# Optimization experiments

Hardware: AMD Instinct MI355X
Metric: run time of the kernel (lower is better)

Reference implementation:

```python
import jax, jax.numpy as jnp
import numpy as np

VOCAB, EMB, HID = 100000, 300, 600
B, S, N = 256, 64, 64
MAX_LEVEL = 3  # depth of the fixed 4-ary tree


def _tree():
    parent = np.zeros(N, np.int32)
    level = np.zeros(N, np.int32)
    for i in range(1, N):
        parent[i] = (i - 1) // 4
        level[i] = level[parent[i]] + 1
    return parent, level


def setup_inputs() -> dict:
    key = jax.random.key(0)
    ks = jax.random.split(key, 16)
    parent, level = _tree()
    E_tab = jax.random.normal(ks[0], (VOCAB, EMB), jnp.float32) * 0.1
    E_tab = E_tab.at[0].set(0.0)  # padding_idx=0
    return dict(
        premise_x=jax.random.randint(ks[1], (B, S), 0, VOCAB),
        hypothesis_x=jax.random.randint(ks[2], (B, S), 0, VOCAB),
        p_word_idx=jax.random.randint(ks[3], (B, N), -1, S),  # -1 => ones vector
        p_rel_id=jax.random.randint(ks[4], (B, N), -1, 4),    # 0..2 transformed, -1/3 identity
        h_word_idx=jax.random.randint(ks[5], (B, N), -1, S),
        h_rel_id=jax.random.randint(ks[6], (B, N), -1, 4),
        parent=jnp.asarray(parent),
        level=jnp.asarray(level),
        E_tab=E_tab,
        W_enc=jax.random.normal(ks[7], (3, EMB, EMB), jnp.float32) * 0.1,
        W0_w=jax.random.normal(ks[8], (HID, 6 * EMB), jnp.float32) * 0.1,
        W0_b=jax.random.normal(ks[9], (HID,), jnp.float32) * 0.1,
        W1_w=jax.random.normal(ks[10], (HID, HID), jnp.float32) * 0.1,
        W1_b=jax.random.normal(ks[11], (HID,), jnp.float32) * 0.1,
        W2_w=jax.random.normal(ks[12], (HID, HID), jnp.float32) * 0.1,
        W2_b=jax.random.normal(ks[13], (HID,), jnp.float32) * 0.1,
        Wout_w=jax.random.normal(ks[14], (3, HID), jnp.float32) * 0.1,
        Wout_b=jax.random.normal(ks[15], (3,), jnp.float32) * 0.1,
    )


def _encode_sg(seq, word_idx, rel_id, parent, level, W_enc):
    # Level-synchronous bottom-up evaluation of: leaf -> word,
    # internal -> relu(word * mean(rel-transformed children)).
    Bn, Nn = word_idx.shape
    Ed = seq.shape[-1]
    idx = jnp.clip(word_idx, 0, None)
    word = jnp.take_along_axis(seq, idx[:, :, None], axis=1)        # [B,N,E]
    word = jnp.where((word_idx == -1)[..., None], 1.0, word)        # word_idx==-1 => ones
    h = word
    pflat = (parent[None, :] + (jnp.arange(Bn) * Nn)[:, None]).reshape(-1)
    for l in range(MAX_LEVEL, 0, -1):
        is_child = jnp.broadcast_to(level[None, :] == l, (Bn, Nn))
        # per-relation linear W_enc[r]: h @ W.T (torch Linear, no bias)
        t_all = jnp.einsum('bne,rfe->bnrf', h, W_enc)               # [B,N,3,E]
        sel = jnp.clip(rel_id, 0, 2)[:, :, None, None]
        t = jnp.take_along_axis(t_all, sel, axis=2)[:, :, 0, :]
        t = jnp.where(((rel_id >= 0) & (rel_id <= 2))[..., None], t, h)
        contrib = jnp.where(is_child[..., None], t, 0.0).reshape(Bn * Nn, Ed)
        sums = jnp.zeros((Bn * Nn, Ed), h.dtype).at[pflat].add(contrib)
        counts = jnp.zeros((Bn * Nn,), h.dtype).at[pflat].add(
            is_child.astype(h.dtype).reshape(-1))
        mean = (sums / jnp.maximum(counts, 1.0)[:, None]).reshape(Bn, Nn, Ed)
        has_child = (counts.reshape(Bn, Nn) > 0)
        h = jnp.where(has_child[..., None], jax.nn.relu(word * mean), h)
    return h[:, 0, :]  # root representation


def reference(premise_x, hypothesis_x, p_word_idx, p_rel_id, h_word_idx, h_rel_id,
              parent, level, E_tab, W_enc, W0_w, W0_b, W1_w, W1_b, W2_w, W2_b,
              Wout_w, Wout_b):
    emb_p = E_tab[premise_x]      # [B,S,E]
    emb_h = E_tab[hypothesis_x]
    p_rep = emb_p.sum(axis=1)
    h_rep = emb_h.sum(axis=1)
    p_sg = _encode_sg(emb_p, p_word_idx, p_rel_id, parent, level, W_enc)
    h_sg = _encode_sg(emb_h, h_word_idx, h_rel_id, parent, level, W_enc)
    x = jnp.concatenate([p_rep, h_rep, p_rep - h_rep, p_rep * h_rep,
                         p_sg - h_sg, p_sg * h_sg], axis=1)  # [B,6E]
    h1 = jax.nn.relu(x @ W0_w.T + W0_b)
    h2 = jax.nn.relu(h1 @ W1_w.T + W1_b)
    h3 = jax.nn.relu(h2 @ W2_w.T + W2_b)
    return h3 @ Wout_w.T + Wout_b  # [B,3]
```

## Files before the change

kernel.cpp:

```cpp
#include <hip/hip_runtime.h>

constexpr int NB = 256;
constexpr int NS = 64;
constexpr int NN = 64;
constexpr int NE = 300;
constexpr int NH = 600;

typedef __attribute__((ext_vector_type(8))) short bf16x8;
typedef __attribute__((ext_vector_type(4))) float f32x4;

constexpr int KT0 = 57;
constexpr int KT1 = 19;
constexpr int NJT = 40;
constexpr int HP  = 640;

constexpr size_t OFF_REP = 0;
constexpr size_t SZ_REP  = (size_t)2*NB*NE;
constexpr size_t OFF_ROOT= OFF_REP + SZ_REP;
constexpr size_t OFF_WBF = OFF_ROOT + SZ_REP;
constexpr size_t SZ_WBF  = (size_t)3*20*10*64*8/2;
constexpr size_t OFF_W0S = OFF_WBF + SZ_WBF;
constexpr size_t SZ_W0S  = (size_t)KT0*NJT*64*8/2;
constexpr size_t OFF_W1S = OFF_W0S + SZ_W0S;
constexpr size_t SZ_W1S  = (size_t)KT1*NJT*64*8/2;
constexpr size_t OFF_W2S = OFF_W1S + SZ_W1S;
constexpr size_t OFF_XSW = OFF_W2S + SZ_W1S;
constexpr size_t SZ_XSW  = (size_t)KT0*16*64*8/2;
constexpr size_t OFF_H1  = OFF_XSW + SZ_XSW;
constexpr size_t SZ_H    = (size_t)NB*HP/2;
constexpr size_t OFF_H2  = OFF_H1 + SZ_H;
constexpr size_t OFF_H3  = OFF_H2 + SZ_H;

__device__ __forceinline__ ushort f2bf(float x) {
  unsigned u = __float_as_uint(x);
  unsigned r = (u + 0x7FFFu + ((u >> 16) & 1u)) >> 16;
  return (ushort)r;
}
__device__ __forceinline__ float bf2f(ushort u) {
  return __uint_as_float(((unsigned)u) << 16);
}

constexpr int NSWZ = 3*20*10*64;
constexpr int N0S  = KT0*NJT*64;
constexpr int N1S  = KT1*NJT*64;
constexpr int SETUP_ITEMS  = NSWZ + N0S + 2*N1S;
constexpr int SETUP_BLOCKS = SETUP_ITEMS/256;

__global__ __launch_bounds__(256)
void k_setup(const float* __restrict__ Wenc, const float* __restrict__ W0,
             const float* __restrict__ W1, const float* __restrict__ W2,
             ushort* __restrict__ Wbf, ushort* __restrict__ W0S,
             ushort* __restrict__ W1S, ushort* __restrict__ W2S) {
  int t = blockIdx.x*256 + threadIdx.x;
  if (t < NSWZ) {
    int lane = t & 63, rest = t >> 6;
    int ksi = rest % 10, rnt = rest / 10, nt = rnt % 20, r = rnt / 20;
    int f = nt*16 + (lane & 15), e0 = ksi*32 + (lane >> 4)*8;
    ushort v[8];
    #pragma unroll
    for (int j = 0; j < 8; j++) {
      int e = e0 + j;
      v[j] = (f < NE && e < NE) ? f2bf(Wenc[((size_t)r*NE + f)*NE + e]) : (ushort)0;
    }
    *reinterpret_cast<int4*>(&Wbf[(size_t)t*8]) = *reinterpret_cast<const int4*>(v);
    return;
  }
  t -= NSWZ;
  const float* W; ushort* D; int K;
  if (t < N0S)              { W = W0; D = W0S; K = 6*NE; }
  else { t -= N0S;
    if (t < N1S)            { W = W1; D = W1S; K = NH; }
    else { t -= N1S;          W = W2; D = W2S; K = NH; } }
  int lane = t & 63, g = t >> 6;
  int jt = g % NJT, kt = g / NJT;
  int j  = jt*16 + (lane & 15);
  int kb = kt*32 + (lane >> 4)*8;
  ushort v[8];
  #pragma unroll
  for (int i = 0; i < 8; i++) {
    int k = kb + i;
    v[i] = (j < NH && k < K) ? f2bf(W[(size_t)j*K + k]) : (ushort)0;
  }
  *reinterpret_cast<int4*>(&D[(size_t)t*8]) = *reinterpret_cast<const int4*>(v);
}

constexpr int TS = 328;

__global__ __launch_bounds__(256)
void k_tree(const int* __restrict__ px, const int* __restrict__ hx,
            const int* __restrict__ pwi, const int* __restrict__ prel,
            const int* __restrict__ hwi, const int* __restrict__ hrel,
            const float* __restrict__ Etab, const ushort* __restrict__ Wbf,
            float* __restrict__ rep, float* __restrict__ root) {
  __shared__ __align__(16) ushort hS[64*TS];
  __shared__ int xsh[64];
  __shared__ int wish[64];
  __shared__ int relsh[64];
  const int sb = blockIdx.x;
  const int s = sb >> 8, b = sb & 255;
  const int tid = threadIdx.x;

  if (tid < 64) xsh[tid] = ((s ? hx : px) + b*NS)[tid];
  else if (tid < 128) wish[tid-64] = ((s ? hwi : pwi) + b*NN)[tid-64];
  else if (tid < 192) relsh[tid-128] = ((s ? hrel : prel) + b*NN)[tid-128];
  __syncthreads();

  for (int e = tid; e < NE; e += 256) {
    float acc = 0.f;
    #pragma unroll 8
    for (int j = 0; j < NS; j++) acc += Etab[(size_t)xsh[j]*NE + e];
    rep[(size_t)sb*NE + e] = acc;
  }
  for (int flat = tid; flat < 64*75; flat += 256) {
    int n = flat / 75, c = flat % 75;
    int w = wish[n];
    float4 v;
    if (w < 0) v = float4{1.f,1.f,1.f,1.f};
    else v = *reinterpret_cast<const float4*>(&Etab[(size_t)xsh[w]*NE + c*4]);
    ushort4 o; o.x = f2bf(v.x); o.y = f2bf(v.y); o.z = f2bf(v.z); o.w = f2bf(v.w);
    *reinterpret_cast<ushort4*>(&hS[n*TS + c*4]) = o;
  }
  for (int z = tid; z < 64*10; z += 256) {
    int row = z / 10, cc = z % 10;
    *reinterpret_cast<unsigned*>(&hS[row*TS + 300 + cc*2]) = 0u;
  }
  __syncthreads();

  const int wave = tid >> 6, lane = tid & 63;
  const int mrow = lane & 15, quad = lane >> 4;

  {
    const int mb0 = 21, mb1 = 37, mb2 = 53;
    bf16x8 af[3][10];
    #pragma unroll
    for (int ks = 0; ks < 10; ks++) {
      af[0][ks] = *reinterpret_cast<const bf16x8*>(&hS[(mb0+mrow)*TS + ks*32 + quad*8]);
      af[1][ks] = *reinterpret_cast<const bf16x8*>(&hS[(mb1+mrow)*TS + ks*32 + quad*8]);
      int r2 = min(mb2+mrow, 63);
      af[2][ks] = *reinterpret_cast<const bf16x8*>(&hS[r2*TS + ks*32 + quad*8]);
    }
    __syncthreads();
    for (int pr = wave; pr < 57; pr += 4) {
      int r = pr / 19, nt = pr % 19;
      const ushort* Wb = &Wbf[(size_t)((r*20 + nt)*10)*64*8];
      f32x4 acc0 = f32x4{0.f,0.f,0.f,0.f};
      f32x4 acc1 = f32x4{0.f,0.f,0.f,0.f};
      f32x4 acc2 = f32x4{0.f,0.f,0.f,0.f};
      #pragma unroll
      for (int ks = 0; ks < 10; ks++) {
        bf16x8 bf = *reinterpret_cast<const bf16x8*>(&Wb[((size_t)ks*64 + lane)*8]);
        acc0 = __builtin_amdgcn_mfma_f32_16x16x32_bf16(af[0][ks], bf, acc0, 0, 0, 0);
        acc1 = __builtin_amdgcn_mfma_f32_16x16x32_bf16(af[1][ks], bf, acc1, 0, 0, 0);
        acc2 = __builtin_amdgcn_mfma_f32_16x16x32_bf16(af[2][ks], bf, acc2, 0, 0, 0);
      }
      int f = nt*16 + mrow;
      if (f < NE) {
        #pragma unroll
        for (int reg = 0; reg < 4; reg++) {
          int m = quad*4 + reg;
          int c0 = mb0 + m, c1 = mb1 + m, c2 = mb2 + m;
          if (relsh[c0] == r) hS[c0*TS + f] = f2bf(acc0[reg]);
          if (relsh[c1] == r) hS[c1*TS + f] = f2bf(acc1[reg]);
          if (c2 < 64 && relsh[c2] == r) hS[c2*TS + f] = f2bf(acc2[reg]);
        }
      }
    }
    __syncthreads();
    for (int f = tid; f < NE; f += 256) {
      #pragma unroll
      for (int p = 5; p <= 15; p++) {
        int nc = (p == 15) ? 3 : 4;
        float sum = 0.f;
        for (int j = 0; j < nc; j++) sum += bf2f(hS[(4*p+1+j)*TS + f]);
        float v = bf2f(hS[p*TS + f]) * sum * (1.0f/(float)nc);
        hS[p*TS + f] = f2bf(v > 0.f ? v : 0.f);
      }
    }
    __syncthreads();
  }

  {
    bf16x8 af[10];
    #pragma unroll
    for (int ks = 0; ks < 10; ks++)
      af[ks] = *reinterpret_cast<const bf16x8*>(&hS[(5+mrow)*TS + ks*32 + quad*8]);
    __syncthreads();
    for (int pr = wave; pr < 57; pr += 4) {
      int r = pr / 19, nt = pr % 19;
      const ushort* Wb = &Wbf[(size_t)((r*20 + nt)*10)*64*8];
      f32x4 acc = f32x4{0.f,0.f,0.f,0.f};
      #pragma unroll
      for (int ks = 0; ks < 10; ks++) {
        bf16x8 bf = *reinterpret_cast<const bf16x8*>(&Wb[((size_t)ks*64 + lane)*8]);
        acc = __builtin_amdgcn_mfma_f32_16x16x32_bf16(af[ks], bf, acc, 0, 0, 0);
      }
      int f = nt*16 + mrow;
      if (f < NE) {
        #pragma unroll
        for (int reg = 0; reg < 4; reg++) {
          int c = 5 + quad*4 + reg;
          if (relsh[c] == r) hS[c*TS + f] = f2bf(acc[reg]);
        }
      }
    }
    __syncthreads();
    for (int f = tid; f < NE; f += 256) {
      #pragma unroll
      for (int p = 1; p <= 4; p++) {
        float sum = 0.f;
        #pragma unroll
        for (int j = 0; j < 4; j++) sum += bf2f(hS[(4*p+1+j)*TS + f]);
        float v = bf2f(hS[p*TS + f]) * sum * 0.25f;
        hS[p*TS + f] = f2bf(v > 0.f ? v : 0.f);
      }
    }
    __syncthreads();
  }

  {
    bool rp0 = (relsh[1]==0)|(relsh[2]==0)|(relsh[3]==0)|(relsh[4]==0);
    bool rp1 = (relsh[1]==1)|(relsh[2]==1)|(relsh[3]==1)|(relsh[4]==1);
    bool rp2 = (relsh[1]==2)|(relsh[2]==2)|(relsh[3]==2)|(relsh[4]==2);
    bf16x8 af[10];
    #pragma unroll
    for (int ks = 0; ks < 10; ks++)
      af[ks] = *reinterpret_cast<const bf16x8*>(&hS[(1+min(mrow,3))*TS + ks*32 + quad*8]);
    __syncthreads();
    for (int pr = wave; pr < 57; pr += 4) {
      int r = pr / 19, nt = pr % 19;
      if ((r==0 && !rp0) || (r==1 && !rp1) || (r==2 && !rp2)) continue;
      const ushort* Wb = &Wbf[(size_t)((r*20 + nt)*10)*64*8];
      f32x4 acc = f32x4{0.f,0.f,0.f,0.f};
      #pragma unroll
      for (int ks = 0; ks < 10; ks++) {
        bf16x8 bf = *reinterpret_cast<const bf16x8*>(&Wb[((size_t)ks*64 + lane)*8]);
        acc = __builtin_amdgcn_mfma_f32_16x16x32_bf16(af[ks], bf, acc, 0, 0, 0);
      }
      int f = nt*16 + mrow;
      if (f < NE) {
        #pragma unroll
        for (int reg = 0; reg < 4; reg++) {
          int m = quad*4 + reg;
          if (m < 4 && relsh[1+m] == r) hS[(1+m)*TS + f] = f2bf(acc[reg]);
        }
      }
    }
    __syncthreads();
    for (int f = tid; f < NE; f += 256) {
      float sum = 0.f;
      #pragma unroll
      for (int c = 1; c <= 4; c++) sum += bf2f(hS[c*TS + f]);
      float v = bf2f(hS[0*TS + f]) * sum * 0.25f;
      root[(size_t)sb*NE + f] = v > 0.f ? v : 0.f;
    }
  }
}

constexpr int FEAT_ITEMS  = KT0*16*64;
constexpr int FEAT_BLOCKS = FEAT_ITEMS/256;

__global__ __launch_bounds__(256)
void k_feat(const float* __restrict__ rep, const float* __restrict__ root,
            ushort* __restrict__ Xsw) {
  int t = blockIdx.x*256 + threadIdx.x;
  int lane = t & 63, g = t >> 6;
  int mt = g % 16, kt = g / 16;
  int b  = mt*16 + (lane & 15);
  int kb = kt*32 + (lane >> 4)*8;
  const float* rp = rep  + (size_t)b*NE;
  const float* rh = rep  + (size_t)(NB+b)*NE;
  const float* tp = root + (size_t)b*NE;
  const float* th = root + (size_t)(NB+b)*NE;
  ushort v[8];
  #pragma unroll
  for (int i = 0; i < 8; i++) {
    int k = kb + i;
    float x = 0.f;
    if (k < 6*NE) {
      int seg = k / NE, e = k - seg*NE;
      switch (seg) {
        case 0:  x = rp[e]; break;
        case 1:  x = rh[e]; break;
        case 2:  x = rp[e] - rh[e]; break;
        case 3:  x = rp[e] * rh[e]; break;
        case 4:  x = tp[e] - th[e]; break;
        default: x = tp[e] * th[e]; break;
      }
    }
    v[i] = f2bf(x);
  }
  *reinterpret_cast<int4*>(&Xsw[(size_t)t*8]) = *reinterpret_cast<const int4*>(v);
}

__device__ __forceinline__ void fc_epi(f32x4 acc, int row, int j,
                                       const float* __restrict__ bias,
                                       ushort* __restrict__ hout) {
  float bj = (j < NH) ? bias[j] : 0.f;
  #pragma unroll
  for (int r = 0; r < 4; r++) {
    float v = acc[r] + bj;
    v = v > 0.f ? v : 0.f;
    if (j < 608) hout[(size_t)(row + r)*HP + j] = f2bf(v);
  }
}

__global__ __launch_bounds__(256)
void k_gemm(const ushort* __restrict__ A, const ushort* __restrict__ Wsw,
            const float* __restrict__ bias, ushort* __restrict__ hout,
            int nstep, int mode) {
  const int tid = threadIdx.x;
  const int wv = tid >> 6, lane = tid & 63;
  const int bx = blockIdx.x, by = blockIdx.y;
  const int b0 = bx*64, j0 = by*64;

  const ushort* ap;
  size_t astride;
  if (mode == 0) {
    ap = A + ((size_t)((size_t)bx*4 + wv)*64 + lane)*8;
    astride = (size_t)16*64*8;
  } else {
    ap = A + (size_t)(b0 + wv*16 + (lane & 15))*HP + (lane >> 4)*8;
    astride = 32;
  }
  const ushort* wp = Wsw + ((size_t)(by*4)*64 + lane)*8;
  constexpr size_t WSTRIDE = (size_t)NJT*64*8;

  f32x4 acc0{0.f,0.f,0.f,0.f}, acc1{0.f,0.f,0.f,0.f};
  f32x4 acc2{0.f,0.f,0.f,0.f}, acc3{0.f,0.f,0.f,0.f};
  for (int t = 0; t < nstep; t++) {
    bf16x8 a  = *reinterpret_cast<const bf16x8*>(ap);
    bf16x8 w0 = *reinterpret_cast<const bf16x8*>(wp);
    bf16x8 w1 = *reinterpret_cast<const bf16x8*>(wp + 512);
    bf16x8 w2 = *reinterpret_cast<const bf16x8*>(wp + 1024);
    bf16x8 w3 = *reinterpret_cast<const bf16x8*>(wp + 1536);
    acc0 = __builtin_amdgcn_mfma_f32_16x16x32_bf16(a, w0, acc0, 0, 0, 0);
    acc1 = __builtin_amdgcn_mfma_f32_16x16x32_bf16(a, w1, acc1, 0, 0, 0);
    acc2 = __builtin_amdgcn_mfma_f32_16x16x32_bf16(a, w2, acc2, 0, 0, 0);
    acc3 = __builtin_amdgcn_mfma_f32_16x16x32_bf16(a, w3, acc3, 0, 0, 0);
    ap += astride;
    wp += WSTRIDE;
  }
  int row = b0 + wv*16 + (lane >> 4)*4;
  int jb  = j0 + (lane & 15);
  fc_epi(acc0, row, jb +  0, bias, hout);
  fc_epi(acc1, row, jb + 16, bias, hout);
  fc_epi(acc2, row, jb + 32, bias, hout);
  fc_epi(acc3, row, jb + 48, bias, hout);
}

__global__ __launch_bounds__(64)
void k_out(const ushort* __restrict__ h3, const float* __restrict__ Wout,
           const float* __restrict__ bout, float* __restrict__ out) {
  int b = blockIdx.x, tid = threadIdx.x;
  float a0 = 0.f, a1 = 0.f, a2 = 0.f;
  for (int k = tid; k < NH; k += 64) {
    float xv = bf2f(h3[(size_t)b*HP + k]);
    a0 += xv * Wout[k];
    a1 += xv * Wout[NH + k];
    a2 += xv * Wout[2*NH + k];
  }
  #pragma unroll
  for (int off = 32; off > 0; off >>= 1) {
    a0 += __shfl_down(a0, off, 64);
    a1 += __shfl_down(a1, off, 64);
    a2 += __shfl_down(a2, off, 64);
  }
  if (tid == 0) {
    out[b*3 + 0] = a0 + bout[0];
    out[b*3 + 1] = a1 + bout[1];
    out[b*3 + 2] = a2 + bout[2];
  }
}

extern "C" void kernel_launch(void* const* d_in, const int* in_sizes, int n_in,
                              void* d_out, int out_size, void* d_ws, size_t ws_size,
                              hipStream_t stream) {
  const int*   px    = (const int*)d_in[0];
  const int*   hx    = (const int*)d_in[1];
  const int*   pwi   = (const int*)d_in[2];
  const int*   prel  = (const int*)d_in[3];
  const int*   hwi   = (const int*)d_in[4];
  const int*   hrel  = (const int*)d_in[5];
  const float* Etab  = (const float*)d_in[8];
  const float* Wenc  = (const float*)d_in[9];
  const float* W0w   = (const float*)d_in[10];
  const float* W0b   = (const float*)d_in[11];
  const float* W1w   = (const float*)d_in[12];
  const float* W1b   = (const float*)d_in[13];
  const float* W2w   = (const float*)d_in[14];
  const float* W2b   = (const float*)d_in[15];
  const float* Woutw = (const float*)d_in[16];
  const float* Woutb = (const float*)d_in[17];

  float* ws   = (float*)d_ws;
  float*  rep  = ws + OFF_REP;
  float*  root = ws + OFF_ROOT;
  ushort* Wbf  = (ushort*)(ws + OFF_WBF);
  ushort* W0S  = (ushort*)(ws + OFF_W0S);
  ushort* W1S  = (ushort*)(ws + OFF_W1S);
  ushort* W2S  = (ushort*)(ws + OFF_W2S);
  ushort* Xsw  = (ushort*)(ws + OFF_XSW);
  ushort* h1   = (ushort*)(ws + OFF_H1);
  ushort* h2   = (ushort*)(ws + OFF_H2);
  ushort* h3   = (ushort*)(ws + OFF_H3);
  float* outp = (float*)d_out;

  dim3 blk(256);
  k_setup<<<dim3(SETUP_BLOCKS), blk, 0, stream>>>(
      Wenc, W0w, W1w, W2w, Wbf, W0S, W1S, W2S);
  k_tree<<<dim3(2*NB), blk, 0, stream>>>(
      px, hx, pwi, prel, hwi, hrel, Etab, Wbf, rep, root);
  k_feat<<<dim3(FEAT_BLOCKS), blk, 0, stream>>>(rep, root, Xsw);
  k_gemm<<<dim3(4,10), blk, 0, stream>>>(Xsw, W0S, W0b, h1, KT0, 0);
  k_gemm<<<dim3(4,10), blk, 0, stream>>>(h1,  W1S, W1b, h2, KT1, 1);
  k_gemm<<<dim3(4,10), blk, 0, stream>>>(h2,  W2S, W2b, h3, KT1, 1);
  k_out<<<dim3(NB), dim3(64), 0, stream>>>(h3, Woutw, Woutb, outp);
}
```

Measured before the change: 314.2 us.

## Fuse feature build, three MLP layers and output head into one kernel

Replaces the feature kernel, the three GEMM launches and the output kernel with a single k_tail kernel. Each block handles 16 batch rows, builds the bf16 feature tile in shared memory in two halves, and keeps the hidden activations in shared memory between layers. This removes four launches and the global round trips for the intermediate activations. In exchange it uses only 16 blocks, each streaming the full weight matrices, so parallelism drops and weight reads are repeated across blocks.

```diff
diff --git a/kernel.cpp b/kernel.cpp
--- a/kernel.cpp
+++ b/kernel.cpp
@@ -12,7 +12,6 @@
 constexpr int KT0 = 57;
 constexpr int KT1 = 19;
 constexpr int NJT = 40;
-constexpr int HP  = 640;
 
 constexpr size_t OFF_REP = 0;
 constexpr size_t SZ_REP  = (size_t)2*NB*NE;
@@ -24,12 +23,6 @@
 constexpr size_t OFF_W1S = OFF_W0S + SZ_W0S;
 constexpr size_t SZ_W1S  = (size_t)KT1*NJT*64*8/2;
 constexpr size_t OFF_W2S = OFF_W1S + SZ_W1S;
-constexpr size_t OFF_XSW = OFF_W2S + SZ_W1S;
-constexpr size_t SZ_XSW  = (size_t)KT0*16*64*8/2;
-constexpr size_t OFF_H1  = OFF_XSW + SZ_XSW;
-constexpr size_t SZ_H    = (size_t)NB*HP/2;
-constexpr size_t OFF_H2  = OFF_H1 + SZ_H;
-constexpr size_t OFF_H3  = OFF_H2 + SZ_H;
 
 __device__ __forceinline__ ushort f2bf(float x) {
   unsigned u = __float_as_uint(x);
@@ -178,7 +171,6 @@
     }
     __syncthreads();
   }
-
   {
     bf16x8 af[10];
     #pragma unroll
@@ -216,7 +208,6 @@
     }
     __syncthreads();
   }
-
   {
     bool rp0 = (relsh[1]==0)|(relsh[2]==0)|(relsh[3]==0)|(relsh[4]==0);
     bool rp1 = (relsh[1]==1)|(relsh[2]==1)|(relsh[3]==1)|(relsh[4]==1);
@@ -256,119 +247,139 @@
   }
 }
 
-constexpr int FEAT_ITEMS  = KT0*16*64;
-constexpr int FEAT_BLOCKS = FEAT_ITEMS/256;
-
-__global__ __launch_bounds__(256)
-void k_feat(const float* __restrict__ rep, const float* __restrict__ root,
-            ushort* __restrict__ Xsw) {
-  int t = blockIdx.x*256 + threadIdx.x;
-  int lane = t & 63, g = t >> 6;
-  int mt = g % 16, kt = g / 16;
-  int b  = mt*16 + (lane & 15);
-  int kb = kt*32 + (lane >> 4)*8;
-  const float* rp = rep  + (size_t)b*NE;
-  const float* rh = rep  + (size_t)(NB+b)*NE;
-  const float* tp = root + (size_t)b*NE;
-  const float* th = root + (size_t)(NB+b)*NE;
-  ushort v[8];
-  #pragma unroll
-  for (int i = 0; i < 8; i++) {
-    int k = kb + i;
-    float x = 0.f;
-    if (k < 6*NE) {
-      int seg = k / NE, e = k - seg*NE;
-      switch (seg) {
-        case 0:  x = rp[e]; break;
-        case 1:  x = rh[e]; break;
-        case 2:  x = rp[e] - rh[e]; break;
-        case 3:  x = rp[e] * rh[e]; break;
-        case 4:  x = tp[e] - th[e]; break;
-        default: x = tp[e] * th[e]; break;
-      }
-    }
-    v[i] = f2bf(x);
-  }
-  *reinterpret_cast<int4*>(&Xsw[(size_t)t*8]) = *reinterpret_cast<const int4*>(v);
-}
-
-__device__ __forceinline__ void fc_epi(f32x4 acc, int row, int j,
-                                       const float* __restrict__ bias,
-                                       ushort* __restrict__ hout) {
-  float bj = (j < NH) ? bias[j] : 0.f;
-  #pragma unroll
-  for (int r = 0; r < 4; r++) {
-    float v = acc[r] + bj;
-    v = v > 0.f ? v : 0.f;
-    if (j < 608) hout[(size_t)(row + r)*HP + j] = f2bf(v);
-  }
-}
-
-__global__ __launch_bounds__(256)
-void k_gemm(const ushort* __restrict__ A, const ushort* __restrict__ Wsw,
-            const float* __restrict__ bias, ushort* __restrict__ hout,
-            int nstep, int mode) {
+constexpr int TB   = 16;
+constexpr int HKT  = 29;
+constexpr int HSTR = 648;
+
+__global__ __launch_bounds__(512)
+void k_tail(const float* __restrict__ rep, const float* __restrict__ root,
+            const ushort* __restrict__ W0S, const ushort* __restrict__ W1S,
+            const ushort* __restrict__ W2S,
+            const float* __restrict__ b0v, const float* __restrict__ b1v,
+            const float* __restrict__ b2v,
+            const float* __restrict__ Woutw, const float* __restrict__ Woutb,
+            float* __restrict__ outp) {
+  __shared__ __align__(16) ushort XA[HKT*64*8];
+  __shared__ __align__(16) ushort HB[TB*HSTR];
   const int tid = threadIdx.x;
   const int wv = tid >> 6, lane = tid & 63;
-  const int bx = blockIdx.x, by = blockIdx.y;
-  const int b0 = bx*64, j0 = by*64;
-
-  const ushort* ap;
-  size_t astride;
-  if (mode == 0) {
-    ap = A + ((size_t)((size_t)bx*4 + wv)*64 + lane)*8;
-    astride = (size_t)16*64*8;
-  } else {
-    ap = A + (size_t)(b0 + wv*16 + (lane & 15))*HP + (lane >> 4)*8;
-    astride = 32;
-  }
-  const ushort* wp = Wsw + ((size_t)(by*4)*64 + lane)*8;
-  constexpr size_t WSTRIDE = (size_t)NJT*64*8;
-
-  f32x4 acc0{0.f,0.f,0.f,0.f}, acc1{0.f,0.f,0.f,0.f};
-  f32x4 acc2{0.f,0.f,0.f,0.f}, acc3{0.f,0.f,0.f,0.f};
-  for (int t = 0; t < nstep; t++) {
-    bf16x8 a  = *reinterpret_cast<const bf16x8*>(ap);
-    bf16x8 w0 = *reinterpret_cast<const bf16x8*>(wp);
-    bf16x8 w1 = *reinterpret_cast<const bf16x8*>(wp + 512);
-    bf16x8 w2 = *reinterpret_cast<const bf16x8*>(wp + 1024);
-    bf16x8 w3 = *reinterpret_cast<const bf16x8*>(wp + 1536);
-    acc0 = __builtin_amdgcn_mfma_f32_16x16x32_bf16(a, w0, acc0, 0, 0, 0);
-    acc1 = __builtin_amdgcn_mfma_f32_16x16x32_bf16(a, w1, acc1, 0, 0, 0);
-    acc2 = __builtin_amdgcn_mfma_f32_16x16x32_bf16(a, w2, acc2, 0, 0, 0);
-    acc3 = __builtin_amdgcn_mfma_f32_16x16x32_bf16(a, w3, acc3, 0, 0, 0);
-    ap += astride;
-    wp += WSTRIDE;
-  }
-  int row = b0 + wv*16 + (lane >> 4)*4;
-  int jb  = j0 + (lane & 15);
-  fc_epi(acc0, row, jb +  0, bias, hout);
-  fc_epi(acc1, row, jb + 16, bias, hout);
-  fc_epi(acc2, row, jb + 32, bias, hout);
-  fc_epi(acc3, row, jb + 48, bias, hout);
-}
-
-__global__ __launch_bounds__(64)
-void k_out(const ushort* __restrict__ h3, const float* __restrict__ Wout,
-           const float* __restrict__ bout, float* __restrict__ out) {
-  int b = blockIdx.x, tid = threadIdx.x;
-  float a0 = 0.f, a1 = 0.f, a2 = 0.f;
-  for (int k = tid; k < NH; k += 64) {
-    float xv = bf2f(h3[(size_t)b*HP + k]);
-    a0 += xv * Wout[k];
-    a1 += xv * Wout[NH + k];
-    a2 += xv * Wout[2*NH + k];
-  }
+  const int b0 = blockIdx.x * TB;
+
+  f32x4 acc[5];
   #pragma unroll
-  for (int off = 32; off > 0; off >>= 1) {
-    a0 += __shfl_down(a0, off, 64);
-    a1 += __shfl_down(a1, off, 64);
-    a2 += __shfl_down(a2, off, 64);
-  }
-  if (tid == 0) {
-    out[b*3 + 0] = a0 + bout[0];
-    out[b*3 + 1] = a1 + bout[1];
-    out[b*3 + 2] = a2 + bout[2];
+  for (int q = 0; q < 5; q++) acc[q] = f32x4{0.f,0.f,0.f,0.f};
+
+  for (int hh = 0; hh < 2; hh++) {
+    const int kbase = hh * HKT;
+    const int nk = hh ? (KT0 - HKT) : HKT;
+    for (int it = tid; it < nk*64; it += 512) {
+      int l = it & 63, ktl = it >> 6;
+      int b = b0 + (l & 15);
+      int kb = (kbase + ktl)*32 + (l >> 4)*8;
+      const float* rp = rep  + (size_t)b*NE;
+      const float* rh = rep  + (size_t)(NB+b)*NE;
+      const float* tp = root + (size_t)b*NE;
+      const float* th = root + (size_t)(NB+b)*NE;
+      ushort v[8];
+      #pragma unroll
+      for (int i = 0; i < 8; i++) {
+        int k = kb + i;
+        float x = 0.f;
+        if (k < 6*NE) {
+          int seg = k / NE, e = k - seg*NE;
+          switch (seg) {
+            case 0:  x = rp[e]; break;
+            case 1:  x = rh[e]; break;
+            case 2:  x = rp[e] - rh[e]; break;
+            case 3:  x = rp[e] * rh[e]; break;
+            case 4:  x = tp[e] - th[e]; break;
+            default: x = tp[e] * th[e]; break;
+          }
+        }
+        v[i] = f2bf(x);
+      }
+      *reinterpret_cast<int4*>(&XA[(size_t)(ktl*64 + l)*8]) =
+          *reinterpret_cast<const int4*>(v);
+    }
+    __syncthreads();
+    for (int ktl = 0; ktl < nk; ktl++) {
+      int kt = kbase + ktl;
+      bf16x8 a = *reinterpret_cast<const bf16x8*>(&XA[(size_t)(ktl*64 + lane)*8]);
+      #pragma unroll
+      for (int q = 0; q < 5; q++) {
+        bf16x8 w = *reinterpret_cast<const bf16x8*>(
+            &W0S[((size_t)(kt*NJT + wv*5 + q)*64 + lane)*8]);
+        acc[q] = __builtin_amdgcn_mfma_f32_16x16x32_bf16(a, w, acc[q], 0, 0, 0);
+      }
+    }
+    __syncthreads();
+  }
+  {
+    int r0 = (lane >> 4)*4;
+    #pragma unroll
+    for (int q = 0; q < 5; q++) {
+      int j = (wv*5 + q)*16 + (lane & 15);
+      if (j < 608) {
+        float bj = (j < 600) ? b0v[j] : 0.f;
+        #pragma unroll
+        for (int r = 0; r < 4; r++) {
+          float vv = acc[q][r] + bj;
+          vv = vv > 0.f ? vv : 0.f;
+          HB[(size_t)(r0 + r)*HSTR + j] = (j < 600) ? f2bf(vv) : (ushort)0;
+        }
+      }
+    }
+  }
+  __syncthreads();
+
+  for (int l = 1; l <= 2; l++) {
+    const ushort* Hs = (l == 1) ? HB : XA;
+    ushort*       Hd = (l == 1) ? XA : HB;
+    const ushort* Ws = (l == 1) ? W1S : W2S;
+    const float*  bs = (l == 1) ? b1v : b2v;
+    #pragma unroll
+    for (int q = 0; q < 5; q++) acc[q] = f32x4{0.f,0.f,0.f,0.f};
+    for (int kt = 0; kt < KT1; kt++) {
+      bf16x8 a = *reinterpret_cast<const bf16x8*>(
+          &Hs[(size_t)(lane & 15)*HSTR + kt*32 + (lane >> 4)*8]);
+      #pragma unroll
+      for (int q = 0; q < 5; q++) {
+        bf16x8 w = *reinterpret_cast<const bf16x8*>(
+            &Ws[((size_t)(kt*NJT + wv*5 + q)*64 + lane)*8]);
+        acc[q] = __builtin_amdgcn_mfma_f32_16x16x32_bf16(a, w, acc[q], 0, 0, 0);
+      }
+    }
+    {
+      int r0 = (lane >> 4)*4;
+      #pragma unroll
+      for (int q = 0; q < 5; q++) {
+        int j = (wv*5 + q)*16 + (lane & 15);
+        if (j < 608) {
+          float bj = (j < 600) ? bs[j] : 0.f;
+          #pragma unroll
+          for (int r = 0; r < 4; r++) {
+            float vv = acc[q][r] + bj;
+            vv = vv > 0.f ? vv : 0.f;
+            Hd[(size_t)(r0 + r)*HSTR + j] = (j < 600) ? f2bf(vv) : (ushort)0;
+          }
+        }
+      }
+    }
+    __syncthreads();
+  }
+
+  {
+    int p = tid >> 3, sub = tid & 7;
+    if (p < TB*3) {
+      int row = p / 3, c = p - row*3;
+      float s = 0.f;
+      for (int k = sub; k < NH; k += 8)
+        s += bf2f(HB[(size_t)row*HSTR + k]) * Woutw[(size_t)c*NH + k];
+      #pragma unroll
+      for (int off = 4; off > 0; off >>= 1)
+        s += __shfl_xor(s, off, 8);
+      if (sub == 0) outp[(size_t)(b0 + row)*3 + c] = s + Woutb[c];
+    }
   }
 }
 
@@ -399,20 +410,12 @@
   ushort* W0S  = (ushort*)(ws + OFF_W0S);
   ushort* W1S  = (ushort*)(ws + OFF_W1S);
   ushort* W2S  = (ushort*)(ws + OFF_W2S);
-  ushort* Xsw  = (ushort*)(ws + OFF_XSW);
-  ushort* h1   = (ushort*)(ws + OFF_H1);
-  ushort* h2   = (ushort*)(ws + OFF_H2);
-  ushort* h3   = (ushort*)(ws + OFF_H3);
   float* outp = (float*)d_out;
 
-  dim3 blk(256);
-  k_setup<<<dim3(SETUP_BLOCKS), blk, 0, stream>>>(
+  k_setup<<<dim3(SETUP_BLOCKS), dim3(256), 0, stream>>>(
       Wenc, W0w, W1w, W2w, Wbf, W0S, W1S, W2S);
-  k_tree<<<dim3(2*NB), blk, 0, stream>>>(
+  k_tree<<<dim3(2*NB), dim3(256), 0, stream>>>(
       px, hx, pwi, prel, hwi, hrel, Etab, Wbf, rep, root);
-  k_feat<<<dim3(FEAT_BLOCKS), blk, 0, stream>>>(rep, root, Xsw);
-  k_gemm<<<dim3(4,10), blk, 0, stream>>>(Xsw, W0S, W0b, h1, KT0, 0);
-  k_gemm<<<dim3(4,10), blk, 0, stream>>>(h1,  W1S, W1b, h2, KT1, 1);
-  k_gemm<<<dim3(4,10), blk, 0, stream>>>(h2,  W2S, W2b, h3, KT1, 1);
-  k_out<<<dim3(NB), dim3(64), 0, stream>>>(h3, Woutw, Woutb, outp);
-}
+  k_tail<<<dim3(NB/TB), dim3(512), 0, stream>>>(
+      rep, root, W0S, W1S, W2S, W0b, W1b, W2b, Woutw, Woutb, outp);
+}
```

Result: slower. 386.0 us (+22.9%).

## Split FC GEMM K-loop across waves with shared-memory reduction

Applied to the files above, without the earlier changes.

Rewrites the three MLP layer kernels so each block covers 16 rows instead of 64 and its four waves split the K dimension, then combine partial accumulators through shared memory before the bias/ReLU epilogue. The grid grows from 40 to 160 blocks, filling more compute units and cutting the serial K-chain each wave walks. In exchange it adds an LDS reduction and a barrier, and weight tiles are now re-read by more blocks.

```diff
diff --git a/kernel.cpp b/kernel.cpp
--- a/kernel.cpp
+++ b/kernel.cpp
@@ -178,7 +178,6 @@
     }
     __syncthreads();
   }
-
   {
     bf16x8 af[10];
     #pragma unroll
@@ -216,7 +215,6 @@
     }
     __syncthreads();
   }
-
   {
     bool rp0 = (relsh[1]==0)|(relsh[2]==0)|(relsh[3]==0)|(relsh[4]==0);
     bool rp1 = (relsh[1]==1)|(relsh[2]==1)|(relsh[3]==1)|(relsh[4]==1);
@@ -292,60 +290,53 @@
   *reinterpret_cast<int4*>(&Xsw[(size_t)t*8]) = *reinterpret_cast<const int4*>(v);
 }
 
-__device__ __forceinline__ void fc_epi(f32x4 acc, int row, int j,
-                                       const float* __restrict__ bias,
-                                       ushort* __restrict__ hout) {
-  float bj = (j < NH) ? bias[j] : 0.f;
-  #pragma unroll
-  for (int r = 0; r < 4; r++) {
-    float v = acc[r] + bj;
-    v = v > 0.f ? v : 0.f;
-    if (j < 608) hout[(size_t)(row + r)*HP + j] = f2bf(v);
-  }
-}
-
 __global__ __launch_bounds__(256)
-void k_gemm(const ushort* __restrict__ A, const ushort* __restrict__ Wsw,
-            const float* __restrict__ bias, ushort* __restrict__ hout,
-            int nstep, int mode) {
-  const int tid = threadIdx.x;
-  const int wv = tid >> 6, lane = tid & 63;
+void k_fc(const ushort* __restrict__ A, const ushort* __restrict__ Wsw,
+          const float* __restrict__ bias, ushort* __restrict__ hout,
+          int nkt, int mode) {
+  __shared__ __align__(16) float red[4*4*64*4];
+  const int tid = threadIdx.x, wv = tid >> 6, lane = tid & 63;
   const int bx = blockIdx.x, by = blockIdx.y;
-  const int b0 = bx*64, j0 = by*64;
-
-  const ushort* ap;
-  size_t astride;
-  if (mode == 0) {
-    ap = A + ((size_t)((size_t)bx*4 + wv)*64 + lane)*8;
-    astride = (size_t)16*64*8;
-  } else {
-    ap = A + (size_t)(b0 + wv*16 + (lane & 15))*HP + (lane >> 4)*8;
-    astride = 32;
-  }
-  const ushort* wp = Wsw + ((size_t)(by*4)*64 + lane)*8;
-  constexpr size_t WSTRIDE = (size_t)NJT*64*8;
-
-  f32x4 acc0{0.f,0.f,0.f,0.f}, acc1{0.f,0.f,0.f,0.f};
-  f32x4 acc2{0.f,0.f,0.f,0.f}, acc3{0.f,0.f,0.f,0.f};
-  for (int t = 0; t < nstep; t++) {
-    bf16x8 a  = *reinterpret_cast<const bf16x8*>(ap);
-    bf16x8 w0 = *reinterpret_cast<const bf16x8*>(wp);
-    bf16x8 w1 = *reinterpret_cast<const bf16x8*>(wp + 512);
-    bf16x8 w2 = *reinterpret_cast<const bf16x8*>(wp + 1024);
-    bf16x8 w3 = *reinterpret_cast<const bf16x8*>(wp + 1536);
-    acc0 = __builtin_amdgcn_mfma_f32_16x16x32_bf16(a, w0, acc0, 0, 0, 0);
-    acc1 = __builtin_amdgcn_mfma_f32_16x16x32_bf16(a, w1, acc1, 0, 0, 0);
-    acc2 = __builtin_amdgcn_mfma_f32_16x16x32_bf16(a, w2, acc2, 0, 0, 0);
-    acc3 = __builtin_amdgcn_mfma_f32_16x16x32_bf16(a, w3, acc3, 0, 0, 0);
-    ap += astride;
-    wp += WSTRIDE;
-  }
-  int row = b0 + wv*16 + (lane >> 4)*4;
-  int jb  = j0 + (lane & 15);
-  fc_epi(acc0, row, jb +  0, bias, hout);
-  fc_epi(acc1, row, jb + 16, bias, hout);
-  fc_epi(acc2, row, jb + 32, bias, hout);
-  fc_epi(acc3, row, jb + 48, bias, hout);
+
+  f32x4 acc[4];
+  #pragma unroll
+  for (int q = 0; q < 4; q++) acc[q] = f32x4{0.f,0.f,0.f,0.f};
+
+  for (int kt = wv; kt < nkt; kt += 4) {
+    bf16x8 a;
+    if (mode == 0)
+      a = *reinterpret_cast<const bf16x8*>(&A[(((size_t)kt*16 + bx)*64 + lane)*8]);
+    else
+      a = *reinterpret_cast<const bf16x8*>(
+          &A[(size_t)(bx*16 + (lane & 15))*HP + kt*32 + (lane >> 4)*8]);
+    #pragma unroll
+    for (int q = 0; q < 4; q++) {
+      bf16x8 w = *reinterpret_cast<const bf16x8*>(
+          &Wsw[(((size_t)kt*NJT + by*4 + q)*64 + lane)*8]);
+      acc[q] = __builtin_amdgcn_mfma_f32_16x16x32_bf16(a, w, acc[q], 0, 0, 0);
+    }
+  }
+  #pragma unroll
+  for (int q = 0; q < 4; q++)
+    *reinterpret_cast<f32x4*>(&red[(((size_t)q*4 + wv)*64 + lane)*4]) = acc[q];
+  __syncthreads();
+  f32x4 s{0.f,0.f,0.f,0.f};
+  #pragma unroll
+  for (int w = 0; w < 4; w++) {
+    f32x4 p = *reinterpret_cast<f32x4*>(&red[(((size_t)wv*4 + w)*64 + lane)*4]);
+    s[0] += p[0]; s[1] += p[1]; s[2] += p[2]; s[3] += p[3];
+  }
+  int row0 = bx*16 + (lane >> 4)*4;
+  int j = (by*4 + wv)*16 + (lane & 15);
+  if (j < 608) {
+    float bj = (j < NH) ? bias[j] : 0.f;
+    #pragma unroll
+    for (int r = 0; r < 4; r++) {
+      float v = s[r] + bj;
+      v = v > 0.f ? v : 0.f;
+      hout[(size_t)(row0 + r)*HP + j] = (j < NH) ? f2bf(v) : (ushort)0;
+    }
+  }
 }
 
 __global__ __launch_bounds__(64)
@@ -405,14 +396,13 @@
   ushort* h3   = (ushort*)(ws + OFF_H3);
   float* outp = (float*)d_out;
 
-  dim3 blk(256);
-  k_setup<<<dim3(SETUP_BLOCKS), blk, 0, stream>>>(
+  k_setup<<<dim3(SETUP_BLOCKS), dim3(256), 0, stream>>>(
       Wenc, W0w, W1w, W2w, Wbf, W0S, W1S, W2S);
-  k_tree<<<dim3(2*NB), blk, 0, stream>>>(
+  k_tree<<<dim3(2*NB), dim3(256), 0, stream>>>(
       px, hx, pwi, prel, hwi, hrel, Etab, Wbf, rep, root);
-  k_feat<<<dim3(FEAT_BLOCKS), blk, 0, stream>>>(rep, root, Xsw);
-  k_gemm<<<dim3(4,10), blk, 0, stream>>>(Xsw, W0S, W0b, h1, KT0, 0);
-  k_gemm<<<dim3(4,10), blk, 0, stream>>>(h1,  W1S, W1b, h2, KT1, 1);
-  k_gemm<<<dim3(4,10), blk, 0, stream>>>(h2,  W2S, W2b, h3, KT1, 1);
+  k_feat<<<dim3(FEAT_BLOCKS), dim3(256), 0, stream>>>(rep, root, Xsw);
+  k_fc<<<dim3(16,10), dim3(256), 0, stream>>>(Xsw, W0S, W0b, h1, KT0, 0);
+  k_fc<<<dim3(16,10), dim3(256), 0, stream>>>(h1,  W1S, W1b, h2, KT1, 1);
+  k_fc<<<dim3(16,10), dim3(256), 0, stream>>>(h2,  W2S, W2b, h3, KT1, 1);
   k_out<<<dim3(NB), dim3(64), 0, stream>>>(h3, Woutw, Woutb, outp);
 }
```

Result: faster. 293.0 us (-6.7%).
